# Performance work log

Measured on AMD Instinct MI355X. Metric: run time of the kernel, lower is better.

The kernel has to match this reference:

```python
import jax, jax.numpy as jnp
import numpy as np

ALPHA = 2.0
MARGIN = 0.05


def setup_inputs() -> dict:
    key = jax.random.key(0)
    k1, k2, k3, k4 = jax.random.split(key, 4)
    B, n_dim, n_classes = 8192, 2048, 100
    x = jax.random.normal(k1, (B, 1, n_dim), dtype=jnp.float32)
    W = jax.random.normal(k2, (n_dim, n_classes), dtype=jnp.float32) * 0.02
    anchors = jax.random.normal(k3, (n_classes, 1, n_dim), dtype=jnp.float32)
    y = jax.random.randint(k4, (B,), 0, n_classes)
    return {"x": x, "W": W, "anchors": anchors, "y": y}


def reference(x, W, anchors, y):
    # x: (B, 1, n_dim), W: (n_dim, C) linear classifier, anchors: (C, 1, n_dim), y: (B,)
    B = x.shape[0]
    n_classes = W.shape[1]
    xf = x.reshape(B, -1)                               # (B, n_dim)
    px = xf @ W                                         # (B, C) logits
    logp = jax.nn.log_softmax(px, axis=-1)
    ce_x = -jnp.take_along_axis(logp, y[:, None], axis=1)[:, 0]   # (B,)
    onehot = jax.nn.one_hot(y, n_classes, dtype=px.dtype)
    # d(sum ce_x)/dx for a linear classifier: (softmax - onehot) @ W^T (create_graph analogue: differentiable)
    grad_x = (jax.nn.softmax(px, axis=-1) - onehot) @ W.T          # (B, n_dim)

    af = anchors.reshape(n_classes, -1)                 # (C, n_dim)
    pa = af @ W                                         # (C, C), targets = arange(C)
    grad_a = (jax.nn.softmax(pa, axis=-1) - jnp.eye(n_classes, dtype=pa.dtype)) @ W.T  # (C, n_dim)

    # get_anchor_batch: detached gather of grad_a by label
    anchor_batch = jax.lax.stop_gradient(grad_a[y])     # (B, n_dim)
    # get_negative_batch (var='all'): for each i, sum of grad_x[j] over j with y_j != y_i (detached)
    cls_sum = jax.ops.segment_sum(grad_x, y, num_segments=n_classes)   # (C, n_dim)
    negative_batch = jax.lax.stop_gradient(grad_x.sum(axis=0) - cls_sum[y])  # (B, n_dim)

    anchor_positive = jnp.sum(grad_x * anchor_batch, axis=-1)        # (B,)
    anchor_negative = jnp.sum(negative_batch * anchor_batch, axis=-1)  # (B,)
    triplet = anchor_negative - anchor_positive + MARGIN
    loss = ce_x + ALPHA * triplet
    return jnp.mean(loss)
```

## Files before the change

kernel.cpp:

```cpp
#include <hip/hip_runtime.h>
#include <math.h>

#define NB      8192
#define ND      2048
#define NC      100
#define NCP     112
#define ALPHA_  2.0f
#define MARGIN_ 0.05f

typedef short bf16x8 __attribute__((ext_vector_type(8)));
typedef float f32x4 __attribute__((ext_vector_type(4)));

static __device__ __forceinline__ unsigned short f2bf(float f) {
  unsigned u = __float_as_uint(f);
  u += 0x7FFFu + ((u >> 16) & 1u);
  return (unsigned short)(u >> 16);
}

__global__ __launch_bounds__(256) void k_prepW(const float* __restrict__ W,
                                               unsigned short* __restrict__ Wtf,
                                               float* __restrict__ zstrip) {
  const int t = threadIdx.x;
  if (blockIdx.x == 0) {
    for (int i = t; i < 384; i += 256) zstrip[i] = 0.f;
  }
  const int f   = blockIdx.x * 256 + t;
  const int ws  = f / 448;
  const int rem = f - ws * 448;
  const int i   = rem >> 6;
  const int l   = rem & 63;
  const int col = i * 16 + (l & 15);
  const int k0  = ws * 32 + (l >> 4) * 8;
  bf16x8 v;
#pragma unroll
  for (int j = 0; j < 8; ++j)
    v[j] = (short)((col < NC) ? f2bf(W[(size_t)(k0 + j) * NC + col]) : 0);
  *(bf16x8*)(Wtf + (size_t)f * 8) = v;
}

__global__ __launch_bounds__(512) void k_prepG(const unsigned short* __restrict__ Wtf,
                                               const float* __restrict__ A,
                                               float* __restrict__ G2,
                                               float* __restrict__ pa2) {
  __shared__ float red[8][8][64];
  const int t    = threadIdx.x;
  const int w    = t >> 6;
  const int lane = t & 63;
  const int ti   = blockIdx.x / 7;
  const int tj   = blockIdx.x % 7;
  const int arow = ti * 16 + (lane & 15);

  f32x4 accG = {0.f, 0.f, 0.f, 0.f};
  f32x4 accP = {0.f, 0.f, 0.f, 0.f};
#pragma unroll
  for (int s = 0; s < 8; ++s) {
    const int ws = w * 8 + s;
    const bf16x8 afr = *(const bf16x8*)(Wtf + (size_t)(ws * 7 + ti) * 512 + lane * 8);
    const bf16x8 bfr = *(const bf16x8*)(Wtf + (size_t)(ws * 7 + tj) * 512 + lane * 8);
    accG = __builtin_amdgcn_mfma_f32_16x16x32_bf16(afr, bfr, accG, 0, 0, 0);
    bf16x8 aa;
    if (arow < NC) {
      const float* __restrict__ ar =
          A + (size_t)arow * ND + ws * 32 + (lane >> 4) * 8;
      const float4 v0 = *(const float4*)(ar);
      const float4 v1 = *(const float4*)(ar + 4);
      aa[0] = (short)f2bf(v0.x); aa[1] = (short)f2bf(v0.y);
      aa[2] = (short)f2bf(v0.z); aa[3] = (short)f2bf(v0.w);
      aa[4] = (short)f2bf(v1.x); aa[5] = (short)f2bf(v1.y);
      aa[6] = (short)f2bf(v1.z); aa[7] = (short)f2bf(v1.w);
    } else {
#pragma unroll
      for (int q = 0; q < 8; ++q) aa[q] = 0;
    }
    accP = __builtin_amdgcn_mfma_f32_16x16x32_bf16(aa, bfr, accP, 0, 0, 0);
  }
#pragma unroll
  for (int rg = 0; rg < 4; ++rg) {
    red[w][rg][lane]     = accG[rg];
    red[w][4 + rg][lane] = accP[rg];
  }
  __syncthreads();
  if (w < 2) {
    const int vb = w * 4;
    float* __restrict__ dst = (w == 0) ? G2 : pa2;
#pragma unroll
    for (int rg = 0; rg < 4; ++rg) {
      float s = 0.f;
#pragma unroll
      for (int w2 = 0; w2 < 8; ++w2) s += red[w2][vb + rg][lane];
      const int row = ti * 16 + (lane >> 4) * 4 + rg;
      dst[row * NCP + tj * 16 + (lane & 15)] = s;
    }
  }
}

__global__ __launch_bounds__(128) void k_prep2(const float* __restrict__ G2,
                                               const float* __restrict__ pa2,
                                               const int* __restrict__ Y,
                                               float* __restrict__ Ut,
                                               int* __restrict__ hist) {
  __shared__ float vals[128];
  __shared__ float tl[128];
  const int cp = blockIdx.x;
  const int t  = threadIdx.x;
  {
    const int i = cp * 82 + t;
    if (t < 82 && i < NB) atomicAdd(&hist[Y[i]], 1);
  }
  const float v = (t < NC) ? pa2[cp * NCP + t] : -INFINITY;
  vals[t] = v;
  __syncthreads();
  float m = -INFINITY;
  for (int c = 0; c < NC; ++c) m = fmaxf(m, vals[c]);
  float se = 0.f;
  for (int c = 0; c < NC; ++c) se += __expf(vals[c] - m);
  tl[t] = (t < NC) ? (__expf(v - m) / se - (t == cp ? 1.f : 0.f)) : 0.f;
  __syncthreads();
  if (t < NC) {
    float u = 0.f;
    for (int c = 0; c < NC; ++c) u = fmaf(G2[c * NCP + t], tl[c], u);
    Ut[cp * NC + t] = u;
  }
}

__global__ __launch_bounds__(512, 4) void k_main(const float* __restrict__ X,
                                                 const unsigned short* __restrict__ Wtf,
                                                 const int* __restrict__ Y,
                                                 const float* __restrict__ Ut,
                                                 float* __restrict__ S_part,
                                                 float* __restrict__ rowce,
                                                 float* __restrict__ rowap) {
  __shared__ __align__(16) char smem[65536];
  const int t    = threadIdx.x;
  const int w    = t >> 6;
  const int lane = t & 63;
  const int row0 = blockIdx.x * 16;
  char* __restrict__ wbase = smem + w * 8192;

  const unsigned short* __restrict__ bp0 =
      Wtf + (size_t)(w * 8 * 7) * 512 + lane * 8;
  bf16x8 cur[7], nxt[7];
#pragma unroll
  for (int i = 0; i < 7; ++i) cur[i] = *(const bf16x8*)(bp0 + i * 512);

  {
    const int srow = lane >> 2;
    const int sc   = lane & 3;
    const float* __restrict__ xr =
        X + (size_t)(row0 + srow) * ND + w * 256 + sc * 8;
    const int wsz = (srow & 7) << 4;
#pragma unroll
    for (int j = 0; j < 8; ++j) {
      const float4 v0 = *(const float4*)(xr + j * 32);
      const float4 v1 = *(const float4*)(xr + j * 32 + 4);
      bf16x8 p;
      p[0] = (short)f2bf(v0.x); p[1] = (short)f2bf(v0.y);
      p[2] = (short)f2bf(v0.z); p[3] = (short)f2bf(v0.w);
      p[4] = (short)f2bf(v1.x); p[5] = (short)f2bf(v1.y);
      p[6] = (short)f2bf(v1.z); p[7] = (short)f2bf(v1.w);
      *(bf16x8*)(wbase + srow * 512 + ((sc * 16 + j * 64) ^ wsz)) = p;
    }
  }

  const int r = lane & 15;
  const int g = lane >> 4;

  f32x4 acc[7];
  const f32x4 z = {0.f, 0.f, 0.f, 0.f};
#pragma unroll
  for (int i = 0; i < 7; ++i) acc[i] = z;

  const char* __restrict__ abase = wbase + r * 512;
  const int asz = (r & 7) << 4;
#pragma unroll
  for (int s = 0; s < 8; ++s) {
    const bf16x8 xf = *(const bf16x8*)(abase + ((s * 64 + g * 16) ^ asz));
    if (s < 7) {
      const unsigned short* __restrict__ bpn = bp0 + (size_t)(s + 1) * 7 * 512;
#pragma unroll
      for (int i = 0; i < 7; ++i) nxt[i] = *(const bf16x8*)(bpn + i * 512);
    }
#pragma unroll
    for (int i = 0; i < 7; ++i)
      acc[i] = __builtin_amdgcn_mfma_f32_16x16x32_bf16(xf, cur[i], acc[i], 0, 0, 0);
#pragma unroll
    for (int i = 0; i < 7; ++i) cur[i] = nxt[i];
  }
  __syncthreads();

  float* __restrict__ redp = (float*)smem;
  float* __restrict__ sp   = (float*)(smem + 57344);
#pragma unroll
  for (int i = 0; i < 7; ++i)
#pragma unroll
    for (int j = 0; j < 4; ++j)
      redp[(w * 7 + i) * 256 + j * 64 + lane] = acc[i][j];
  if (t < NCP) sp[t] = 0.f;
  __syncthreads();

  if (w < 4) {
    const int j = w;
    float v[7];
#pragma unroll
    for (int i = 0; i < 7; ++i) {
      float s = 0.f;
#pragma unroll
      for (int w2 = 0; w2 < 8; ++w2)
        s += redp[(w2 * 7 + i) * 256 + j * 64 + lane];
      v[i] = s;
    }
    const bool v6  = (96 + r) < NC;
    const int  row = row0 + g * 4 + j;
    const int  yr  = Y[row];

    float m = -INFINITY;
#pragma unroll
    for (int i = 0; i < 6; ++i) m = fmaxf(m, v[i]);
    if (v6) m = fmaxf(m, v[6]);
#pragma unroll
    for (int off = 8; off > 0; off >>= 1) m = fmaxf(m, __shfl_xor(m, off));

    float e[7];
    float se = 0.f, py = 0.f;
#pragma unroll
    for (int i = 0; i < 7; ++i) {
      const bool valid = (i < 6) | v6;
      e[i] = valid ? __expf(v[i] - m) : 0.f;
      se += e[i];
      if (i * 16 + r == yr) py = v[i];
    }
#pragma unroll
    for (int off = 8; off > 0; off >>= 1) {
      se += __shfl_xor(se, off);
      py += __shfl_xor(py, off);
    }
    const float ce  = m + __logf(se) - py;
    const float inv = 1.f / se;

    const float* __restrict__ uty = Ut + yr * NC;
    float ap = 0.f;
    float s[7];
#pragma unroll
    for (int i = 0; i < 7; ++i) {
      const int col = i * 16 + r;
      s[i] = e[i] * inv - (col == yr ? 1.f : 0.f);
      const float u = ((i < 6) | v6) ? uty[col] : 0.f;
      ap = fmaf(s[i], u, ap);
    }
#pragma unroll
    for (int off = 8; off > 0; off >>= 1) ap += __shfl_xor(ap, off);

    if (r == 0) {
      rowce[row] = ce;
      rowap[row] = ap;
    }
#pragma unroll
    for (int i = 0; i < 7; ++i) atomicAdd(&sp[i * 16 + r], s[i]);
  }
  __syncthreads();
  if (t < NCP) S_part[(size_t)t * 512 + blockIdx.x] = sp[t];
}

__global__ __launch_bounds__(256) void k_red(const int* __restrict__ Y,
                                             const float* __restrict__ S_part,
                                             const float* __restrict__ rowce,
                                             const float* __restrict__ rowap,
                                             float* __restrict__ stot,
                                             float* __restrict__ sums,
                                             float* __restrict__ cls_ap) {
  __shared__ float red[256];
  __shared__ float clsap[128];
  const int bid = blockIdx.x;
  const int t   = threadIdx.x;
  if (bid < NCP) {
    red[t] = S_part[(size_t)bid * 512 + t] + S_part[(size_t)bid * 512 + 256 + t];
    __syncthreads();
    for (int off = 128; off > 0; off >>= 1) {
      if (t < off) red[t] += red[t + off];
      __syncthreads();
    }
    if (t == 0) stot[bid] = red[0];
  } else {
    const int base = (bid - NCP) * 512;
    if (t < 128) clsap[t] = 0.f;
    __syncthreads();
    float ces = 0.f, aps = 0.f;
#pragma unroll
    for (int q = 0; q < 2; ++q) {
      const int i = base + q * 256 + t;
      const float a = rowap[i];
      ces += rowce[i];
      aps += a;
      atomicAdd(&clsap[Y[i]], a);
    }
    red[t] = ces;
    __syncthreads();
    for (int off = 128; off > 0; off >>= 1) {
      if (t < off) red[t] += red[t + off];
      __syncthreads();
    }
    if (t == 0) atomicAdd(&sums[0], red[0]);
    __syncthreads();
    red[t] = aps;
    __syncthreads();
    for (int off = 128; off > 0; off >>= 1) {
      if (t < off) red[t] += red[t + off];
      __syncthreads();
    }
    if (t == 0) atomicAdd(&sums[1], red[0]);
    if (t < NC) atomicAdd(&cls_ap[t], clsap[t]);
  }
}

__global__ __launch_bounds__(256) void k_final(const int* __restrict__ hist,
                                               const float* __restrict__ Ut,
                                               const float* __restrict__ stot,
                                               const float* __restrict__ sums,
                                               const float* __restrict__ cls_ap,
                                               float* __restrict__ out) {
  __shared__ float st[NC];
  __shared__ float red2[256];
  const int t = threadIdx.x;
  if (t < NC) st[t] = stot[t];
  __syncthreads();
  float part = 0.f;
  if (t < NC) {
    float dot = 0.f;
    for (int c = 0; c < NC; ++c) dot = fmaf(st[c], Ut[t * NC + c], dot);
    part = (float)hist[t] * (dot - cls_ap[t]);
  }
  red2[t] = part;
  __syncthreads();
  for (int off = 128; off > 0; off >>= 1) {
    if (t < off) red2[t] += red2[t + off];
    __syncthreads();
  }
  if (t == 0) {
    out[0] = (sums[0] + ALPHA_ * (red2[0] - sums[1] + (float)NB * MARGIN_)) /
             (float)NB;
  }
}

extern "C" void kernel_launch(void* const* d_in, const int* in_sizes, int n_in,
                              void* d_out, int out_size, void* d_ws,
                              size_t ws_size, hipStream_t stream) {
  const float* X = (const float*)d_in[0];
  const float* W = (const float*)d_in[1];
  const float* A = (const float*)d_in[2];
  const int*   Y = (const int*)d_in[3];
  float* out = (float*)d_out;
  char*  ws  = (char*)d_ws;

  float*          G2     = (float*)(ws + 0);
  float*          pa2    = (float*)(ws + 50176);
  float*          Ut     = (float*)(ws + 100352);
  float*          cls_ap = (float*)(ws + 140800);
  int*            hist   = (int*)(ws + 141312);
  float*          sums   = (float*)(ws + 141824);
  float*          stot   = (float*)(ws + 142336);
  unsigned short* Wtf    = (unsigned short*)(ws + 147456);
  float*          S_part = (float*)(ws + 606208);
  float*          rowce  = (float*)(ws + 835584);
  float*          rowap  = (float*)(ws + 868352);

  k_prepW<<<112, 256, 0, stream>>>(W, Wtf, cls_ap);
  k_prepG<<<49, 512, 0, stream>>>(Wtf, A, G2, pa2);
  k_prep2<<<NC, 128, 0, stream>>>(G2, pa2, Y, Ut, hist);
  k_main<<<NB / 16, 512, 0, stream>>>(X, Wtf, Y, Ut, S_part, rowce, rowap);
  k_red<<<128, 256, 0, stream>>>(Y, S_part, rowce, rowap, stot, sums, cls_ap);
  k_final<<<1, 256, 0, stream>>>(hist, Ut, stot, sums, cls_ap, out);
}
```

Before: 60.09 us.

## Split logits GEMM by class tile per wave instead of K-split with reduction

The k_main logits GEMM is repartitioned. Before, each of the 8 waves covered a K-slice for all 7 class tiles, and the partial sums were combined through shared memory. Now each of 7 waves owns one 16-column class tile over the full K range, reading X rows that all waves staged into padded shared memory. This removes the 8-way cross-wave reduction and puts the prepared W in class-tile-major order (grid resized to 128 blocks), but one wave sits idle during the GEMM, each wave runs a longer dependent MFMA chain on a single accumulator, and shared memory grows to about 73 KB, which may limit occupancy.

```diff
diff --git a/kernel.cpp b/kernel.cpp
--- a/kernel.cpp
+++ b/kernel.cpp
@@ -17,17 +17,18 @@
   return (unsigned short)(u >> 16);
 }
 
+
 __global__ __launch_bounds__(256) void k_prepW(const float* __restrict__ W,
-                                               unsigned short* __restrict__ Wtf,
+                                               unsigned short* __restrict__ Wtf8,
                                                float* __restrict__ zstrip) {
   const int t = threadIdx.x;
   if (blockIdx.x == 0) {
     for (int i = t; i < 384; i += 256) zstrip[i] = 0.f;
   }
-  const int f   = blockIdx.x * 256 + t;
-  const int ws  = f / 448;
-  const int rem = f - ws * 448;
-  const int i   = rem >> 6;
+  const int c   = blockIdx.x * 256 + t;
+  const int i   = c >> 12;
+  const int rem = c & 4095;
+  const int ws  = rem >> 6;
   const int l   = rem & 63;
   const int col = i * 16 + (l & 15);
   const int k0  = ws * 32 + (l >> 4) * 8;
@@ -35,10 +36,10 @@
 #pragma unroll
   for (int j = 0; j < 8; ++j)
     v[j] = (short)((col < NC) ? f2bf(W[(size_t)(k0 + j) * NC + col]) : 0);
-  *(bf16x8*)(Wtf + (size_t)f * 8) = v;
-}
-
-__global__ __launch_bounds__(512) void k_prepG(const unsigned short* __restrict__ Wtf,
+  *(bf16x8*)(Wtf8 + (size_t)c * 8) = v;
+}
+
+__global__ __launch_bounds__(512) void k_prepG(const unsigned short* __restrict__ Wtf8,
                                                const float* __restrict__ A,
                                                float* __restrict__ G2,
                                                float* __restrict__ pa2) {
@@ -55,8 +56,8 @@
 #pragma unroll
   for (int s = 0; s < 8; ++s) {
     const int ws = w * 8 + s;
-    const bf16x8 afr = *(const bf16x8*)(Wtf + (size_t)(ws * 7 + ti) * 512 + lane * 8);
-    const bf16x8 bfr = *(const bf16x8*)(Wtf + (size_t)(ws * 7 + tj) * 512 + lane * 8);
+    const bf16x8 afr = *(const bf16x8*)(Wtf8 + (size_t)(ti * 64 + ws) * 512 + lane * 8);
+    const bf16x8 bfr = *(const bf16x8*)(Wtf8 + (size_t)(tj * 64 + ws) * 512 + lane * 8);
     accG = __builtin_amdgcn_mfma_f32_16x16x32_bf16(afr, bfr, accG, 0, 0, 0);
     bf16x8 aa;
     if (arow < NC) {
@@ -124,24 +125,21 @@
 }
 
 __global__ __launch_bounds__(512, 4) void k_main(const float* __restrict__ X,
-                                                 const unsigned short* __restrict__ Wtf,
+                                                 const unsigned short* __restrict__ Wtf8,
                                                  const int* __restrict__ Y,
                                                  const float* __restrict__ Ut,
                                                  float* __restrict__ S_part,
                                                  float* __restrict__ rowce,
                                                  float* __restrict__ rowap) {
-  __shared__ __align__(16) char smem[65536];
+  __shared__ __align__(16) char smem[74752];
   const int t    = threadIdx.x;
   const int w    = t >> 6;
   const int lane = t & 63;
   const int row0 = blockIdx.x * 16;
-  char* __restrict__ wbase = smem + w * 8192;
-
-  const unsigned short* __restrict__ bp0 =
-      Wtf + (size_t)(w * 8 * 7) * 512 + lane * 8;
-  bf16x8 cur[7], nxt[7];
-#pragma unroll
-  for (int i = 0; i < 7; ++i) cur[i] = *(const bf16x8*)(bp0 + i * 512);
+  const int r    = lane & 15;
+  const int g    = lane >> 4;
+  float* __restrict__ px = (float*)(smem + 65792);
+  float* __restrict__ sp = (float*)(smem + 74240);
 
   {
     const int srow = lane >> 2;
@@ -149,6 +147,7 @@
     const float* __restrict__ xr =
         X + (size_t)(row0 + srow) * ND + w * 256 + sc * 8;
     const int wsz = (srow & 7) << 4;
+    char* __restrict__ rbase = smem + srow * 4112 + w * 512;
 #pragma unroll
     for (int j = 0; j < 8; ++j) {
       const float4 v0 = *(const float4*)(xr + j * 32);
@@ -158,57 +157,49 @@
       p[2] = (short)f2bf(v0.z); p[3] = (short)f2bf(v0.w);
       p[4] = (short)f2bf(v1.x); p[5] = (short)f2bf(v1.y);
       p[6] = (short)f2bf(v1.z); p[7] = (short)f2bf(v1.w);
-      *(bf16x8*)(wbase + srow * 512 + ((sc * 16 + j * 64) ^ wsz)) = p;
-    }
-  }
-
-  const int r = lane & 15;
-  const int g = lane >> 4;
-
-  f32x4 acc[7];
-  const f32x4 z = {0.f, 0.f, 0.f, 0.f};
-#pragma unroll
-  for (int i = 0; i < 7; ++i) acc[i] = z;
-
-  const char* __restrict__ abase = wbase + r * 512;
-  const int asz = (r & 7) << 4;
-#pragma unroll
-  for (int s = 0; s < 8; ++s) {
-    const bf16x8 xf = *(const bf16x8*)(abase + ((s * 64 + g * 16) ^ asz));
-    if (s < 7) {
-      const unsigned short* __restrict__ bpn = bp0 + (size_t)(s + 1) * 7 * 512;
-#pragma unroll
-      for (int i = 0; i < 7; ++i) nxt[i] = *(const bf16x8*)(bpn + i * 512);
-    }
-#pragma unroll
-    for (int i = 0; i < 7; ++i)
-      acc[i] = __builtin_amdgcn_mfma_f32_16x16x32_bf16(xf, cur[i], acc[i], 0, 0, 0);
-#pragma unroll
-    for (int i = 0; i < 7; ++i) cur[i] = nxt[i];
-  }
-  __syncthreads();
-
-  float* __restrict__ redp = (float*)smem;
-  float* __restrict__ sp   = (float*)(smem + 57344);
-#pragma unroll
-  for (int i = 0; i < 7; ++i)
-#pragma unroll
-    for (int j = 0; j < 4; ++j)
-      redp[(w * 7 + i) * 256 + j * 64 + lane] = acc[i][j];
+      *(bf16x8*)(rbase + ((sc * 16 + j * 64) ^ wsz)) = p;
+    }
+  }
   if (t < NCP) sp[t] = 0.f;
+  __syncthreads();
+
+  if (w < 7) {
+    f32x4 acc = {0.f, 0.f, 0.f, 0.f};
+    const unsigned short* __restrict__ bp = Wtf8 + (size_t)w * 32768 + lane * 8;
+    const char* __restrict__ arow_base = smem + r * 4112;
+    const int asz = (r & 7) << 4;
+    bf16x8 bufA[4], bufB[4];
+#pragma unroll
+    for (int u = 0; u < 4; ++u) bufA[u] = *(const bf16x8*)(bp + u * 512);
+#pragma unroll
+    for (int sb = 0; sb < 16; ++sb) {
+      if (sb < 15) {
+#pragma unroll
+        for (int u = 0; u < 4; ++u)
+          bufB[u] = *(const bf16x8*)(bp + ((sb + 1) * 4 + u) * 512);
+      }
+#pragma unroll
+      for (int u = 0; u < 4; ++u) {
+        const int s = sb * 4 + u;
+        const bf16x8 a = *(const bf16x8*)(
+            arow_base + (s >> 3) * 512 + ((((s & 7) * 64) + g * 16) ^ asz));
+        acc = __builtin_amdgcn_mfma_f32_16x16x32_bf16(a, bufA[u], acc, 0, 0, 0);
+      }
+#pragma unroll
+      for (int u = 0; u < 4; ++u) bufA[u] = bufB[u];
+    }
+#pragma unroll
+    for (int jr = 0; jr < 4; ++jr)
+      px[(g * 4 + jr) * 132 + w * 16 + r] = acc[jr];
+  }
   __syncthreads();
 
   if (w < 4) {
     const int j = w;
     float v[7];
 #pragma unroll
-    for (int i = 0; i < 7; ++i) {
-      float s = 0.f;
-#pragma unroll
-      for (int w2 = 0; w2 < 8; ++w2)
-        s += redp[(w2 * 7 + i) * 256 + j * 64 + lane];
-      v[i] = s;
-    }
+    for (int i = 0; i < 7; ++i) v[i] = px[(g * 4 + j) * 132 + i * 16 + r];
+
     const bool v6  = (96 + r) < NC;
     const int  row = row0 + g * 4 + j;
     const int  yr  = Y[row];
@@ -358,15 +349,15 @@
   int*            hist   = (int*)(ws + 141312);
   float*          sums   = (float*)(ws + 141824);
   float*          stot   = (float*)(ws + 142336);
-  unsigned short* Wtf    = (unsigned short*)(ws + 147456);
-  float*          S_part = (float*)(ws + 606208);
-  float*          rowce  = (float*)(ws + 835584);
-  float*          rowap  = (float*)(ws + 868352);
-
-  k_prepW<<<112, 256, 0, stream>>>(W, Wtf, cls_ap);
-  k_prepG<<<49, 512, 0, stream>>>(Wtf, A, G2, pa2);
+  unsigned short* Wtf8   = (unsigned short*)(ws + 147456);
+  float*          S_part = (float*)(ws + 671744);
+  float*          rowce  = (float*)(ws + 901120);
+  float*          rowap  = (float*)(ws + 933888);
+
+  k_prepW<<<128, 256, 0, stream>>>(W, Wtf8, cls_ap);
+  k_prepG<<<49, 512, 0, stream>>>(Wtf8, A, G2, pa2);
   k_prep2<<<NC, 128, 0, stream>>>(G2, pa2, Y, Ut, hist);
-  k_main<<<NB / 16, 512, 0, stream>>>(X, Wtf, Y, Ut, S_part, rowce, rowap);
+  k_main<<<NB / 16, 512, 0, stream>>>(X, Wtf8, Y, Ut, S_part, rowce, rowap);
   k_red<<<128, 256, 0, stream>>>(Y, S_part, rowce, rowap, stot, sums, cls_ap);
   k_final<<<1, 256, 0, stream>>>(hist, Ut, stot, sums, cls_ap, out);
 }
```

Result: slower. 62.68 us (+4.3%).
